# Performance work log

Measured on AMD Instinct MI355X. Metric: run time of the kernel, lower is better.

The kernel has to match this reference:

```python
import jax, jax.numpy as jnp
import numpy as np
from jax import lax


def _conv(x, w, b, pad, dil):
    # standard NCHW conv, OIHW weights
    y = lax.conv_general_dilated(x, w, (1, 1), [(pad, pad), (pad, pad)],
                                 rhs_dilation=(dil, dil),
                                 dimension_numbers=('NCHW', 'OIHW', 'NCHW'))
    return y + b[None, :, None, None]


def _bilinear(img, py, px):
    # img: [B,C,H,W]; py,px: [B,KK,H,W] float sample positions.
    # Zero-padding bilinear sampling (torchvision deform_conv semantics):
    # each of the 4 corners contributes 0 if it lies outside the image.
    B, C, H, W = img.shape
    y0 = jnp.floor(py)
    x0 = jnp.floor(px)
    wy1 = py - y0
    wx1 = px - x0
    imgf = img.reshape(B, C, H * W)

    def corner(yi, xi, wgt):
        valid = (yi >= 0) & (yi <= H - 1) & (xi >= 0) & (xi <= W - 1)
        yc = jnp.clip(yi, 0, H - 1).astype(jnp.int32)
        xc = jnp.clip(xi, 0, W - 1).astype(jnp.int32)
        idx = yc * W + xc  # [B,KK,H,W]
        g = jax.vmap(lambda im, ix: jnp.take(im, ix.reshape(-1), axis=1))(imgf, idx)
        g = g.reshape(B, C, *yi.shape[1:])  # [B,C,KK,H,W]
        return g * (wgt * valid.astype(img.dtype))[:, None]

    return (corner(y0, x0, (1 - wy1) * (1 - wx1))
            + corner(y0, x0 + 1, (1 - wy1) * wx1)
            + corner(y0 + 1, x0, wy1 * (1 - wx1))
            + corner(y0 + 1, x0 + 1, wy1 * wx1))


def _deform_dw(x, off_w, off_b, dw_w, K, pad, dil):
    # offset-predicted deformable depthwise conv (groups == channels)
    B, C, H, W = x.shape
    off = _conv(x, off_w, off_b, pad, dil).reshape(B, K * K, 2, H, W)
    dy, dx = off[:, :, 0], off[:, :, 1]  # torchvision order: (dy, dx) per tap
    ky, kx = jnp.meshgrid(jnp.arange(K), jnp.arange(K), indexing='ij')
    by = (ky.reshape(-1) * dil - pad).astype(x.dtype)  # [KK]
    bx = (kx.reshape(-1) * dil - pad).astype(x.dtype)
    py = jnp.arange(H, dtype=x.dtype)[None, None, :, None] + by[None, :, None, None] + dy
    px = jnp.arange(W, dtype=x.dtype)[None, None, None, :] + bx[None, :, None, None] + dx
    s = _bilinear(x, py, px)  # [B,C,KK,H,W]
    return jnp.einsum('bckhw,ck->bchw', s, dw_w.reshape(C, K * K))


def setup_inputs() -> dict:
    key = jax.random.key(0)
    ks = jax.random.split(key, 9)
    B, C, H, W = 4, 64, 56, 56
    f = lambda k, shape, s: jax.random.normal(k, shape, jnp.float32) * s
    return dict(
        x=f(ks[0], (B, C, H, W), 1.0),
        off_w1=f(ks[1], (2 * 5 * 5, C, 5, 5), 0.01), off_b1=f(ks[2], (2 * 5 * 5,), 0.01),
        dw_w1=f(ks[3], (C, 1, 5, 5), 0.1),
        off_w2=f(ks[4], (2 * 7 * 7, C, 7, 7), 0.01), off_b2=f(ks[5], (2 * 7 * 7,), 0.01),
        dw_w2=f(ks[6], (C, 1, 7, 7), 0.1),
        pw_w=f(ks[7], (C, C, 1, 1), 0.05), pw_b=f(ks[8], (C,), 0.05),
    )


def reference(x, off_w1, off_b1, dw_w1, off_w2, off_b2, dw_w2, pw_w, pw_b):
    attn = _deform_dw(x, off_w1, off_b1, dw_w1, 5, 2, 1)       # 5x5 deformable dw
    attn = _deform_dw(attn, off_w2, off_b2, dw_w2, 7, 9, 3)    # 7x7 dil-3 deformable dw
    attn = _conv(attn, pw_w, pw_b, 0, 1)                       # 1x1 pointwise
    return x * attn                                            # gated multiply
```

## Files before the change

kernel.cpp:

```cpp
#include <hip/hip_runtime.h>

#define BB 4
#define CC 64
#define HH 56
#define WW 56
#define HW (HH*WW)

typedef unsigned short u16;
typedef unsigned int u32;
typedef __attribute__((ext_vector_type(8))) short bf16x8;
typedef __attribute__((ext_vector_type(4))) float f32x4;

__device__ __forceinline__ u16 f2bf(float f) {
    union { float f; unsigned u; } c; c.f = f;
    unsigned u = c.u;
    u = (u + 0x7FFFu + ((u >> 16) & 1u)) >> 16;
    return (u16)u;
}
__device__ __forceinline__ float bf2f(u16 v) {
    union { unsigned u; float f; } c; c.u = ((unsigned)v) << 16;
    return c.f;
}
__device__ __forceinline__ float lo_f(u32 u) {
    union { unsigned u; float f; } c; c.u = u << 16; return c.f;
}
__device__ __forceinline__ float hi_f(u32 u) {
    union { unsigned u; float f; } c; c.u = u & 0xffff0000u; return c.f;
}

#define R1 102400
#define R2 401408
#define R3 4096
#define R4 1600
#define R5 3136
#define TGRID (BB*(HW/64))
#define PREPN (R1+R2+R3+R4+R5)
__global__ __launch_bounds__(256)
void prep_tr_kernel(const float* __restrict__ x,
                    const float* __restrict__ ow1, const float* __restrict__ ow2,
                    const float* __restrict__ pw,  const float* __restrict__ dw1,
                    const float* __restrict__ dw2,
                    u16* __restrict__ xT,
                    u16* __restrict__ w2t1, u16* __restrict__ w2t2,
                    u16* __restrict__ pwT, float* __restrict__ dwT1,
                    float* __restrict__ dwT2) {
    __shared__ u16 tile[64][72];
    const int t = threadIdx.x;
    if (blockIdx.x < TGRID) {
        const int blk = blockIdx.x;
        const int b   = blk / (HW/64);
        const int p0  = (blk % (HW/64))*64;
        const int px  = t & 63, icq = t >> 6;
        const float* ip = x + ((size_t)b*CC + icq*16)*HW + p0 + px;
        #pragma unroll
        for (int i = 0; i < 16; ++i)
            tile[px][icq*16 + i] = f2bf(ip[(size_t)i*HW]);
        __syncthreads();
        const int px2 = t >> 2, g = t & 3;
        u16* op = xT + ((size_t)b*HW + p0 + px2)*64 + g*16;
        const uint4* s = (const uint4*)&tile[px2][g*16];
        ((uint4*)op)[0] = s[0];
        ((uint4*)op)[1] = s[1];
        return;
    }
    const int i = (blockIdx.x - TGRID)*256 + t;
    if (i < R1) {
        const int ic = i & 63, n = (i >> 6) & 63, tap = i >> 12;
        w2t1[i] = f2bf((n < 50) ? ow1[((size_t)n*64 + ic)*25 + tap] : 0.f);
    } else if (i < R1+R2) {
        const int j = i - R1;
        const int ic = j & 63, n = (j >> 6) & 127, tap = j >> 13;
        w2t2[j] = f2bf((n < 98) ? ow2[((size_t)n*64 + ic)*49 + tap] : 0.f);
    } else if (i < R1+R2+R3) {
        const int j = i - (R1+R2);
        pwT[j] = f2bf(pw[j]);
    } else if (i < R1+R2+R3+R4) {
        const int j = i - (R1+R2+R3);
        const int c = j & 63, k = j >> 6;
        dwT1[j] = dw1[c*25 + k];
    } else if (i < R1+R2+R3+R4+R5) {
        const int j = i - (R1+R2+R3+R4);
        const int c = j & 63, k = j >> 6;
        dwT2[j] = dw2[c*49 + k];
    }
}

__device__ __forceinline__ uint4 selz(bool v, uint4 a) {
    const uint4 z = make_uint4(0,0,0,0);
    return v ? a : z;
}

template<int K, int DIL, int PAD, int COUT, int NP, int NPAD, int NTW, int NREAL>
__global__ __launch_bounds__(256, 4)
void conv_mfma_lds_kernel(const u16* __restrict__ xT, const u16* __restrict__ w2t,
                          const float* __restrict__ bias, float* __restrict__ out) {
    constexpr int KK = K*K;
    constexpr int BROWS = 16*NTW;
    __shared__ u16 Ab[2][64*64];
    __shared__ u16 Bb[2][BROWS*64];

    const int nm   = HW/64;
    const int b    = blockIdx.x / nm;
    const int p0   = (blockIdx.x % nm)*64;
    const int nt0  = blockIdx.y;
    const int t    = threadIdx.x;
    const int wave = t >> 6;
    const int lane = t & 63;

    const int spx = t >> 3;
    const int sc  = t & 7;
    const int pA  = p0 + spx;
    const int pB  = p0 + spx + 32;
    const int pyA = pA / WW, pxA = pA % WW;
    const int pyB = pB / WW, pxB = pB % WW;
    const u16* xb = xT + (size_t)b*HW*64;
    const int sslotA = ((sc + spx) & 7)*8;
    const int bn  = t >> 3;
    const int bslot = ((sc + bn) & 7)*8;
    const u16* wbase = w2t + (size_t)nt0*BROWS*64;
    const bool bactive = (BROWS == 32 || bn < BROWS) && (nt0*BROWS + bn < NREAL);

    const int r = lane & 15, quad = lane >> 4;
    const int mloc = wave*16 + r;
    const int arow = mloc*64;
    const int a0s = ((quad     + mloc) & 7)*8;
    const int a1s = ((quad + 4 + mloc) & 7)*8;
    const int b0s = ((quad     + r) & 7)*8;
    const int b1s = ((quad + 4 + r) & 7)*8;

    f32x4 acc[NTW];
    #pragma unroll
    for (int h = 0; h < NTW; ++h) acc[h] = (f32x4){0.f,0.f,0.f,0.f};
    const uint4 z4 = make_uint4(0,0,0,0);

    auto LD = [&](int tap, uint4& a0, uint4& a1, bool& va, bool& vb, uint4& bb) {
        const int dyy = (tap/K)*DIL - PAD;
        const int dxx = (tap%K)*DIL - PAD;
        const int off = dyy*WW + dxx;
        {
            const int yy = pyA + dyy, xx = pxA + dxx;
            va = ((unsigned)yy < (unsigned)HH) && ((unsigned)xx < (unsigned)WW);
            a0 = *(const uint4*)(xb + (size_t)(va ? (pA + off) : 0)*64 + sc*8);
        }
        {
            const int yy = pyB + dyy, xx = pxB + dxx;
            vb = ((unsigned)yy < (unsigned)HH) && ((unsigned)xx < (unsigned)WW);
            a1 = *(const uint4*)(xb + (size_t)(vb ? (pB + off) : 0)*64 + sc*8);
        }
        if (bactive)
            bb = *(const uint4*)(wbase + ((size_t)tap*NP + bn)*64 + sc*8);
    };

    uint4 rA0 = z4, rA1 = z4, rB = z4;
    bool v0 = false, v1 = false;
    LD(0, rA0, rA1, v0, v1, rB);

    #pragma unroll
    for (int tap = 0; tap < KK; ++tap) {
        uint4 nA0 = z4, nA1 = z4, nB = z4;
        bool nv0 = false, nv1 = false;
        if (tap + 1 < KK) LD(tap + 1, nA0, nA1, nv0, nv1, nB);

        u16* A  = &Ab[tap & 1][0];
        u16* Bq = &Bb[tap & 1][0];
        *(uint4*)(A + spx*64      + sslotA) = selz(v0, rA0);
        *(uint4*)(A + (spx+32)*64 + sslotA) = selz(v1, rA1);
        if (bactive) *(uint4*)(Bq + bn*64 + bslot) = rB;
        __syncthreads();

        const bf16x8 av0 = *(const bf16x8*)(A + arow + a0s);
        const bf16x8 av1 = *(const bf16x8*)(A + arow + a1s);
        #pragma unroll
        for (int h = 0; h < NTW; ++h) {
            if (NREAL < NP && nt0*BROWS + h*16 >= NREAL) break;
            const int brow = (h*16 + r)*64;
            const bf16x8 bv0 = *(const bf16x8*)(Bq + brow + b0s);
            const bf16x8 bv1 = *(const bf16x8*)(Bq + brow + b1s);
            acc[h] = __builtin_amdgcn_mfma_f32_16x16x32_bf16(av0, bv0, acc[h], 0, 0, 0);
            acc[h] = __builtin_amdgcn_mfma_f32_16x16x32_bf16(av1, bv1, acc[h], 0, 0, 0);
        }

        rA0 = nA0; rA1 = nA1; rB = nB; v0 = nv0; v1 = nv1;
    }

    #pragma unroll
    for (int h = 0; h < NTW; ++h) {
        const int n = nt0*BROWS + h*16 + r;
        if (n < COUT) {
            const float bv = bias[n];
            float* op = out + ((size_t)b*HW + p0 + wave*16 + quad*4)*NPAD + n;
            #pragma unroll
            for (int r2 = 0; r2 < 4; ++r2) op[(size_t)r2*NPAD] = acc[h][r2] + bv;
        }
    }
}

template<int K, int DIL, int PAD, int NPAD>
__global__ __launch_bounds__(128)
void deform_cl_kernel(const u16* __restrict__ inT, const float* __restrict__ offT,
                      const float* __restrict__ dwT, u16* __restrict__ outT) {
    constexpr int KK = K*K;
    constexpr int PXB = 16;
    __shared__ float4 swt[PXB][KK];
    __shared__ int4   sat[PXB][KK];
    __shared__ float  sdw[KK*64];

    const int t = threadIdx.x;
    const int nbX = (BB*HW/PXB) >> 3;
    const int blk0 = blockIdx.x;
    const int blk = (blk0 & 7)*nbX + (blk0 >> 3);
    const int p0 = blk*PXB;
    const int b  = p0 / HW;
    const int pl0 = p0 - b*HW;

    for (int i = t; i < KK*64; i += 128) sdw[i] = dwT[i];

    for (int i = t; i < PXB*KK; i += 128) {
        const int pix = i / KK, k = i - pix*KK;
        const int pl  = pl0 + pix;
        const int h = pl / WW, w = pl % WW;
        const float* orow = offT + ((size_t)b*HW + pl)*NPAD;
        const float dy = orow[2*k];
        const float dx = orow[2*k+1];
        const float py = (float)(h + (k/K)*DIL - PAD) + dy;
        const float px = (float)(w + (k%K)*DIL - PAD) + dx;
        const float y0f = floorf(py), x0f = floorf(px);
        const float wy1 = py - y0f,  wx1 = px - x0f;
        const float wy0 = 1.f - wy1, wx0 = 1.f - wx1;
        const int y0 = (int)y0f, x0 = (int)x0f;

        const int y0c = min(max(y0,   0), HH-1);
        const int y1c = min(max(y0+1, 0), HH-1);
        const int x0c = min(max(x0,   0), WW-1);
        const int x1c = min(max(x0+1, 0), WW-1);
        const float gy0 = wy0 * ((y0   >= 0 && y0   < HH) ? 1.f : 0.f);
        const float gy1 = wy1 * ((y0+1 >= 0 && y0+1 < HH) ? 1.f : 0.f);
        const float gx0 = wx0 * ((x0   >= 0 && x0   < WW) ? 1.f : 0.f);
        const float gx1 = wx1 * ((x0+1 >= 0 && x0+1 < WW) ? 1.f : 0.f);

        swt[pix][k] = make_float4(gy0*gx0, gy0*gx1, gy1*gx0, gy1*gx1);
        const int r0 = y0c*WW, r1 = y1c*WW;
        sat[pix][k] = make_int4((r0 + x0c) << 7, (r0 + x1c) << 7,
                                (r1 + x0c) << 7, (r1 + x1c) << 7);
    }
    __syncthreads();

    const int lane = t & 63, wave = t >> 6;
    const int pix  = wave*8 + (lane >> 3);
    const int cq   = lane & 7;
    const char* ib = (const char*)(inT + (size_t)b*HW*64) + cq*16;

    float acc[8];
    #pragma unroll
    for (int j = 0; j < 8; ++j) acc[j] = 0.f;

    #pragma unroll 4
    for (int k = 0; k < KK; ++k) {
        const float4 wv = swt[pix][k];
        const int4   av = sat[pix][k];
        const uint4 c00 = *(const uint4*)(ib + av.x);
        const uint4 c01 = *(const uint4*)(ib + av.y);
        const uint4 c10 = *(const uint4*)(ib + av.z);
        const uint4 c11 = *(const uint4*)(ib + av.w);
        const float4 d0 = *(const float4*)&sdw[k*64 + cq*8];
        const float4 d1 = *(const float4*)&sdw[k*64 + cq*8 + 4];
        const float dv[8] = {d0.x,d0.y,d0.z,d0.w,d1.x,d1.y,d1.z,d1.w};
        const u32* p00 = (const u32*)&c00;
        const u32* p01 = (const u32*)&c01;
        const u32* p10 = (const u32*)&c10;
        const u32* p11 = (const u32*)&c11;
        #pragma unroll
        for (int j = 0; j < 4; ++j) {
            const u32 u00 = p00[j], u01 = p01[j], u10 = p10[j], u11 = p11[j];
            const float slo = lo_f(u00)*wv.x + lo_f(u01)*wv.y + lo_f(u10)*wv.z + lo_f(u11)*wv.w;
            const float shi = hi_f(u00)*wv.x + hi_f(u01)*wv.y + hi_f(u10)*wv.z + hi_f(u11)*wv.w;
            acc[2*j]   += slo * dv[2*j];
            acc[2*j+1] += shi * dv[2*j+1];
        }
    }

    uint4 ov;
    u32* ow = (u32*)&ov;
    #pragma unroll
    for (int j = 0; j < 4; ++j)
        ow[j] = (u32)f2bf(acc[2*j]) | ((u32)f2bf(acc[2*j+1]) << 16);
    *(uint4*)((char*)outT + (size_t)(p0 + pix)*128 + cq*16) = ov;
}

__global__ __launch_bounds__(256)
void pw_mfma_kernel(const u16* __restrict__ a2T, const u16* __restrict__ pwT,
                    const float* __restrict__ pb, const float* __restrict__ x,
                    float* __restrict__ out) {
    const int nm = HW/64;
    const int b  = blockIdx.x / nm;
    const int p0 = (blockIdx.x % nm)*64 + (threadIdx.x >> 6)*16;
    const int nt = blockIdx.y;
    const int lane = threadIdx.x & 63;
    const int r = lane & 15, quad = lane >> 4;

    const u16* ap = a2T + ((size_t)b*HW + p0 + r)*64 + quad*8;
    f32x4 acc = (f32x4){0.f,0.f,0.f,0.f};
    #pragma unroll
    for (int ks = 0; ks < 2; ++ks) {
        const bf16x8 av = *(const bf16x8*)(ap + ks*32);
        const bf16x8 bv = *(const bf16x8*)(pwT + ((size_t)(nt*16 + r))*64 + ks*32 + quad*8);
        acc = __builtin_amdgcn_mfma_f32_16x16x32_bf16(av, bv, acc, 0, 0, 0);
    }

    const int n = nt*16 + r;
    const float bv = pb[n];
    const size_t base = ((size_t)b*CC + n)*HW + p0 + quad*4;
    #pragma unroll
    for (int r2 = 0; r2 < 4; ++r2)
        out[base + r2] = x[base + r2] * (acc[r2] + bv);
}

template<int K, int DIL, int PAD, int COUT, int OCB>
__global__ __launch_bounds__(256)
void off_conv_sg_kernel(const float* __restrict__ in, const float* __restrict__ wgt,
                        const float* __restrict__ bias, float* __restrict__ out) {
    constexpr int KK = K*K;
    const int nOB = COUT / OCB;
    const int b   = blockIdx.x / nOB;
    const int oc0 = (blockIdx.x % nOB) * OCB;
    const int x   = threadIdx.x;
    const int h   = blockIdx.y*4 + threadIdx.y;

    float acc[OCB];
    #pragma unroll
    for (int o = 0; o < OCB; ++o) acc[o] = bias[oc0+o];

    const float* inb = in + (size_t)b*CC*HW;
    const float* wb  = wgt + (size_t)oc0*CC*KK;

    for (int ic = 0; ic < CC; ++ic) {
        const float* inp = inb + ic*HW;
        const float* wp  = wb + ic*KK;
        #pragma unroll
        for (int ky = 0; ky < K; ++ky) {
            const int  y  = h + ky*DIL - PAD;
            const bool yv = (y >= 0) && (y < HH);
            const int  yc = yv ? y : 0;
            const float* row = inp + yc*WW;
            #pragma unroll
            for (int kx = 0; kx < K; ++kx) {
                const int  xx = x + kx*DIL - PAD;
                const bool v  = yv && (xx >= 0) && (xx < WW);
                const int  xc = (xx < 0) ? 0 : ((xx >= WW) ? (WW-1) : xx);
                float val = row[xc];
                val = v ? val : 0.f;
                const int t = ky*K + kx;
                #pragma unroll
                for (int o = 0; o < OCB; ++o)
                    acc[o] += wp[(size_t)o*CC*KK + t] * val;
            }
        }
    }

    if (x >= WW) return;
    #pragma unroll
    for (int o = 0; o < OCB; ++o)
        out[((size_t)b*COUT + oc0 + o)*HW + h*WW + x] = acc[o];
}

template<int K, int DIL, int PAD>
__global__ __launch_bounds__(64)
void deform_dw_full_kernel(const float* __restrict__ in, const float* __restrict__ off,
                           const float* __restrict__ dw, float* __restrict__ out) {
    constexpr int KK = K*K;
    const int idx = blockIdx.x*64 + threadIdx.x;
    const int x = idx % WW;
    const int h = (idx / WW) % HH;
    const int c = (idx / HW) % CC;
    const int b = idx / (CC*HW);

    const float* inp  = in  + ((size_t)b*CC + c)*HW;
    const float* offp = off + (size_t)b*(2*KK)*HW + h*WW + x;
    const float* dwp  = dw  + c*KK;

    float acc = 0.f;
    #pragma unroll 7
    for (int k = 0; k < KK; ++k) {
        const float dy = offp[(2*k  )*HW];
        const float dx = offp[(2*k+1)*HW];
        const float py = (float)(h + (k/K)*DIL - PAD) + dy;
        const float px = (float)(x + (k%K)*DIL - PAD) + dx;
        const float y0f = floorf(py), x0f = floorf(px);
        const float wy1 = py - y0f,  wx1 = px - x0f;
        const float wy0 = 1.f - wy1, wx0 = 1.f - wx1;
        const int y0 = (int)y0f, x0 = (int)x0f;

        const int y0c = min(max(y0,   0), HH-1);
        const int y1c = min(max(y0+1, 0), HH-1);
        const int x0c = min(max(x0,   0), WW-1);
        const int x1c = min(max(x0+1, 0), WW-1);
        const float my0 = (y0   >= 0 && y0   < HH) ? 1.f : 0.f;
        const float my1 = (y0+1 >= 0 && y0+1 < HH) ? 1.f : 0.f;
        const float mx0 = (x0   >= 0 && x0   < WW) ? 1.f : 0.f;
        const float mx1 = (x0+1 >= 0 && x0+1 < WW) ? 1.f : 0.f;

        const float v00 = inp[y0c*WW + x0c];
        const float v01 = inp[y0c*WW + x1c];
        const float v10 = inp[y1c*WW + x0c];
        const float v11 = inp[y1c*WW + x1c];

        const float gx0 = wx0*mx0, gx1 = wx1*mx1;
        const float s = (v00*gx0 + v01*gx1) * (wy0*my0)
                      + (v10*gx0 + v11*gx1) * (wy1*my1);
        acc += s * dwp[k];
    }
    out[idx] = acc;
}

__global__ __launch_bounds__(256)
void pw_mul_kernel(const float* __restrict__ x, const float* __restrict__ a2,
                   const float* __restrict__ pw, const float* __restrict__ pb,
                   float* __restrict__ out) {
    constexpr int HW4 = HW/4;
    const int t = blockIdx.x*256 + threadIdx.x;
    if (t >= BB*CC*HW4) return;
    const int sp4 = t % HW4;
    const int oc  = (t / HW4) % CC;
    const int b   = t / (CC*HW4);

    const float4* ap = (const float4*)(a2 + (size_t)b*CC*HW) + sp4;
    const float4* wp4 = (const float4*)(pw + oc*CC);
    const float pbv = pb[oc];
    float4 acc = make_float4(pbv, pbv, pbv, pbv);
    #pragma unroll 4
    for (int ic4 = 0; ic4 < CC/4; ++ic4) {
        const float4 w = wp4[ic4];
        float4 a0 = ap[(ic4*4+0)*HW4];
        float4 a1 = ap[(ic4*4+1)*HW4];
        float4 a2v = ap[(ic4*4+2)*HW4];
        float4 a3 = ap[(ic4*4+3)*HW4];
        acc.x += w.x*a0.x + w.y*a1.x + w.z*a2v.x + w.w*a3.x;
        acc.y += w.x*a0.y + w.y*a1.y + w.z*a2v.y + w.w*a3.y;
        acc.z += w.x*a0.z + w.y*a1.z + w.z*a2v.z + w.w*a3.z;
        acc.w += w.x*a0.w + w.y*a1.w + w.z*a2v.w + w.w*a3.w;
    }
    const float4 xv = ((const float4*)x)[t];
    float4 r;
    r.x = xv.x*acc.x; r.y = xv.y*acc.y; r.z = xv.z*acc.z; r.w = xv.w*acc.w;
    ((float4*)out)[t] = r;
}

extern "C" void kernel_launch(void* const* d_in, const int* in_sizes, int n_in,
                              void* d_out, int out_size, void* d_ws, size_t ws_size,
                              hipStream_t stream) {
    const float* x      = (const float*)d_in[0];
    const float* off_w1 = (const float*)d_in[1];
    const float* off_b1 = (const float*)d_in[2];
    const float* dw_w1  = (const float*)d_in[3];
    const float* off_w2 = (const float*)d_in[4];
    const float* off_b2 = (const float*)d_in[5];
    const float* dw_w2  = (const float*)d_in[6];
    const float* pw_w   = (const float*)d_in[7];
    const float* pw_b   = (const float*)d_in[8];
    float* out = (float*)d_out;

    const size_t nF    = (size_t)BB*CC*HW;
    const size_t attnB = nF*sizeof(float);
    const size_t off2B = (size_t)BB*98*HW*sizeof(float);
    const size_t offTB = (size_t)BB*HW*112*sizeof(float);
    const size_t chB   = (size_t)BB*HW*64*sizeof(u16);
    char* ws = (char*)d_ws;

    const int n    = (int)nF;
    const int dbl  = n/64;
    const int pbl  = (n/4 + 255)/256;
    dim3 cblk(64,4);
    dim3 rgrd1(BB*(50/5), HH/4);
    dim3 rgrd2(BB*(98/7), HH/4);
    dim3 cgrd1(TGRID, 2);
    dim3 cgrd2(TGRID, 4);
    dim3 pgrd(TGRID, 4);
    const int dgrid = BB*HW/16;

    const size_t oOFF  = 0;
    const size_t oXT   = oOFF + offTB;
    const size_t oA1T  = oXT  + chB;
    const size_t oA2T  = oA1T + chB;
    const size_t oW1   = oA2T + chB;
    const size_t oW2   = oW1  + (size_t)R1*2;
    const size_t oPWT  = oW2  + (size_t)R2*2;
    const size_t oDW1  = oPWT + (size_t)R3*2;
    const size_t oDW2  = oDW1 + (size_t)R4*4;
    const size_t TOT   = oDW2 + (size_t)R5*4;

    if (ws_size >= TOT) {
        float* off_buf = (float*)(ws + oOFF);
        u16*   xT      = (u16*)(ws + oXT);
        u16*   a1T     = (u16*)(ws + oA1T);
        u16*   a2T     = (u16*)(ws + oA2T);
        u16*   w2t1    = (u16*)(ws + oW1);
        u16*   w2t2    = (u16*)(ws + oW2);
        u16*   pwT     = (u16*)(ws + oPWT);
        float* dwT1    = (float*)(ws + oDW1);
        float* dwT2    = (float*)(ws + oDW2);

        prep_tr_kernel<<<TGRID + (PREPN+255)/256, 256, 0, stream>>>(
            x, off_w1, off_w2, pw_w, dw_w1, dw_w2,
            xT, w2t1, w2t2, pwT, dwT1, dwT2);

        conv_mfma_lds_kernel<5,1,2,50,64,64,2,64><<<cgrd1, 256, 0, stream>>>(xT, w2t1, off_b1, off_buf);
        deform_cl_kernel<5,1,2,64><<<dgrid, 128, 0, stream>>>(xT, off_buf, dwT1, a1T);

        conv_mfma_lds_kernel<7,3,9,98,128,112,2,112><<<cgrd2, 256, 0, stream>>>(a1T, w2t2, off_b2, off_buf);
        deform_cl_kernel<7,3,9,112><<<dgrid, 128, 0, stream>>>(a1T, off_buf, dwT2, a2T);

        pw_mfma_kernel<<<pgrd, 256, 0, stream>>>(a2T, pwT, pw_b, x, out);
    } else if (ws_size >= off2B + attnB) {
        float* off_buf = (float*)ws;
        float* attn1   = (float*)d_out;
        float* attn2   = (float*)(ws + off2B);
        off_conv_sg_kernel<5,1,2,50,5><<<rgrd1, cblk, 0, stream>>>(x, off_w1, off_b1, off_buf);
        deform_dw_full_kernel<5,1,2><<<dbl, 64, 0, stream>>>(x, off_buf, dw_w1, attn1);
        off_conv_sg_kernel<7,3,9,98,7><<<rgrd2, cblk, 0, stream>>>(attn1, off_w2, off_b2, off_buf);
        deform_dw_full_kernel<7,3,9><<<dbl, 64, 0, stream>>>(attn1, off_buf, dw_w2, attn2);
        pw_mul_kernel<<<pbl, 256, 0, stream>>>(x, attn2, pw_w, pw_b, out);
    } else {
        float* attn1 = (float*)d_out;
        float* attn2 = (float*)ws;
        float* off1  = (float*)ws;
        off_conv_sg_kernel<5,1,2,50,5><<<rgrd1, cblk, 0, stream>>>(x, off_w1, off_b1, off1);
        deform_dw_full_kernel<5,1,2><<<dbl, 64, 0, stream>>>(x, off1, dw_w1, attn1);
        float* off2 = (float*)(ws + attnB);
        off_conv_sg_kernel<7,3,9,98,7><<<rgrd2, cblk, 0, stream>>>(attn1, off_w2, off_b2, off2);
        deform_dw_full_kernel<7,3,9><<<dbl, 64, 0, stream>>>(attn1, off2, dw_w2, attn2);
        pw_mul_kernel<<<pbl, 256, 0, stream>>>(x, attn2, pw_w, pw_b, out);
    }
}
```

Before: 165.1 us.

## Double-buffer per-row bilinear setup in deformable kernel with larger blocks

New measurement: 193.0 us. +16.9%, slower.

```diff
diff --git a/kernel.cpp b/kernel.cpp
--- a/kernel.cpp
+++ b/kernel.cpp
@@ -196,13 +196,15 @@
 }
 
 template<int K, int DIL, int PAD, int NPAD>
-__global__ __launch_bounds__(128)
+__global__ __launch_bounds__(256, 4)
 void deform_cl_kernel(const u16* __restrict__ inT, const float* __restrict__ offT,
                       const float* __restrict__ dwT, u16* __restrict__ outT) {
     constexpr int KK = K*K;
-    constexpr int PXB = 16;
-    __shared__ float4 swt[PXB][KK];
-    __shared__ int4   sat[PXB][KK];
+    constexpr int TC = K;
+    constexpr int NC = K;
+    constexpr int PXB = 32;
+    __shared__ float4 swt[2][PXB*TC];
+    __shared__ int4   sat[2][PXB*TC];
     __shared__ float  sdw[KK*64];
 
     const int t = threadIdx.x;
@@ -213,36 +215,42 @@
     const int b  = p0 / HW;
     const int pl0 = p0 - b*HW;
 
-    for (int i = t; i < KK*64; i += 128) sdw[i] = dwT[i];
-
-    for (int i = t; i < PXB*KK; i += 128) {
-        const int pix = i / KK, k = i - pix*KK;
-        const int pl  = pl0 + pix;
-        const int h = pl / WW, w = pl % WW;
-        const float* orow = offT + ((size_t)b*HW + pl)*NPAD;
-        const float dy = orow[2*k];
-        const float dx = orow[2*k+1];
-        const float py = (float)(h + (k/K)*DIL - PAD) + dy;
-        const float px = (float)(w + (k%K)*DIL - PAD) + dx;
-        const float y0f = floorf(py), x0f = floorf(px);
-        const float wy1 = py - y0f,  wx1 = px - x0f;
-        const float wy0 = 1.f - wy1, wx0 = 1.f - wx1;
-        const int y0 = (int)y0f, x0 = (int)x0f;
-
-        const int y0c = min(max(y0,   0), HH-1);
-        const int y1c = min(max(y0+1, 0), HH-1);
-        const int x0c = min(max(x0,   0), WW-1);
-        const int x1c = min(max(x0+1, 0), WW-1);
-        const float gy0 = wy0 * ((y0   >= 0 && y0   < HH) ? 1.f : 0.f);
-        const float gy1 = wy1 * ((y0+1 >= 0 && y0+1 < HH) ? 1.f : 0.f);
-        const float gx0 = wx0 * ((x0   >= 0 && x0   < WW) ? 1.f : 0.f);
-        const float gx1 = wx1 * ((x0+1 >= 0 && x0+1 < WW) ? 1.f : 0.f);
-
-        swt[pix][k] = make_float4(gy0*gx0, gy0*gx1, gy1*gx0, gy1*gx1);
-        const int r0 = y0c*WW, r1 = y1c*WW;
-        sat[pix][k] = make_int4((r0 + x0c) << 7, (r0 + x1c) << 7,
-                                (r1 + x0c) << 7, (r1 + x1c) << 7);
-    }
+    for (int i = t; i < KK*64; i += 256) sdw[i] = dwT[i];
+
+    auto STAGE = [&](int c) {
+        const int i = t;
+        if (i < PXB*TC) {
+            const int pix = i / TC, kk = i - pix*TC;
+            const int k = c*TC + kk;
+            const int pl  = pl0 + pix;
+            const int h = pl / WW, w = pl % WW;
+            const float* orow = offT + ((size_t)b*HW + pl)*NPAD;
+            const float dy = orow[2*k];
+            const float dx = orow[2*k+1];
+            const float py = (float)(h + (k/K)*DIL - PAD) + dy;
+            const float px = (float)(w + (k%K)*DIL - PAD) + dx;
+            const float y0f = floorf(py), x0f = floorf(px);
+            const float wy1 = py - y0f,  wx1 = px - x0f;
+            const float wy0 = 1.f - wy1, wx0 = 1.f - wx1;
+            const int y0 = (int)y0f, x0 = (int)x0f;
+
+            const int y0c = min(max(y0,   0), HH-1);
+            const int y1c = min(max(y0+1, 0), HH-1);
+            const int x0c = min(max(x0,   0), WW-1);
+            const int x1c = min(max(x0+1, 0), WW-1);
+            const float gy0 = wy0 * ((y0   >= 0 && y0   < HH) ? 1.f : 0.f);
+            const float gy1 = wy1 * ((y0+1 >= 0 && y0+1 < HH) ? 1.f : 0.f);
+            const float gx0 = wx0 * ((x0   >= 0 && x0   < WW) ? 1.f : 0.f);
+            const float gx1 = wx1 * ((x0+1 >= 0 && x0+1 < WW) ? 1.f : 0.f);
+
+            swt[c & 1][pix*TC + kk] = make_float4(gy0*gx0, gy0*gx1, gy1*gx0, gy1*gx1);
+            const int r0 = y0c*WW, r1 = y1c*WW;
+            sat[c & 1][pix*TC + kk] = make_int4((r0 + x0c) << 7, (r0 + x1c) << 7,
+                                                (r1 + x0c) << 7, (r1 + x1c) << 7);
+        }
+    };
+
+    STAGE(0);
     __syncthreads();
 
     const int lane = t & 63, wave = t >> 6;
@@ -254,29 +262,36 @@
     #pragma unroll
     for (int j = 0; j < 8; ++j) acc[j] = 0.f;
 
-    #pragma unroll 4
-    for (int k = 0; k < KK; ++k) {
-        const float4 wv = swt[pix][k];
-        const int4   av = sat[pix][k];
-        const uint4 c00 = *(const uint4*)(ib + av.x);
-        const uint4 c01 = *(const uint4*)(ib + av.y);
-        const uint4 c10 = *(const uint4*)(ib + av.z);
-        const uint4 c11 = *(const uint4*)(ib + av.w);
-        const float4 d0 = *(const float4*)&sdw[k*64 + cq*8];
-        const float4 d1 = *(const float4*)&sdw[k*64 + cq*8 + 4];
-        const float dv[8] = {d0.x,d0.y,d0.z,d0.w,d1.x,d1.y,d1.z,d1.w};
-        const u32* p00 = (const u32*)&c00;
-        const u32* p01 = (const u32*)&c01;
-        const u32* p10 = (const u32*)&c10;
-        const u32* p11 = (const u32*)&c11;
+    for (int c = 0; c < NC; ++c) {
+        if (c + 1 < NC) STAGE(c + 1);
+        const float4* wrow = &swt[c & 1][pix*TC];
+        const int4*   arow = &sat[c & 1][pix*TC];
         #pragma unroll
-        for (int j = 0; j < 4; ++j) {
-            const u32 u00 = p00[j], u01 = p01[j], u10 = p10[j], u11 = p11[j];
-            const float slo = lo_f(u00)*wv.x + lo_f(u01)*wv.y + lo_f(u10)*wv.z + lo_f(u11)*wv.w;
-            const float shi = hi_f(u00)*wv.x + hi_f(u01)*wv.y + hi_f(u10)*wv.z + hi_f(u11)*wv.w;
-            acc[2*j]   += slo * dv[2*j];
-            acc[2*j+1] += shi * dv[2*j+1];
-        }
+        for (int kk = 0; kk < TC; ++kk) {
+            const float4 wv = wrow[kk];
+            const int4   av = arow[kk];
+            const uint4 c00 = *(const uint4*)(ib + av.x);
+            const uint4 c01 = *(const uint4*)(ib + av.y);
+            const uint4 c10 = *(const uint4*)(ib + av.z);
+            const uint4 c11 = *(const uint4*)(ib + av.w);
+            const int k = c*TC + kk;
+            const float4 d0 = *(const float4*)&sdw[k*64 + cq*8];
+            const float4 d1 = *(const float4*)&sdw[k*64 + cq*8 + 4];
+            const float dv[8] = {d0.x,d0.y,d0.z,d0.w,d1.x,d1.y,d1.z,d1.w};
+            const u32* p00 = (const u32*)&c00;
+            const u32* p01 = (const u32*)&c01;
+            const u32* p10 = (const u32*)&c10;
+            const u32* p11 = (const u32*)&c11;
+            #pragma unroll
+            for (int j = 0; j < 4; ++j) {
+                const u32 u00 = p00[j], u01 = p01[j], u10 = p10[j], u11 = p11[j];
+                const float slo = lo_f(u00)*wv.x + lo_f(u01)*wv.y + lo_f(u10)*wv.z + lo_f(u11)*wv.w;
+                const float shi = hi_f(u00)*wv.x + hi_f(u01)*wv.y + hi_f(u10)*wv.z + hi_f(u11)*wv.w;
+                acc[2*j]   += slo * dv[2*j];
+                acc[2*j+1] += shi * dv[2*j+1];
+            }
+        }
+        __syncthreads();
     }
 
     uint4 ov;
@@ -475,7 +490,7 @@
     dim3 cgrd1(TGRID, 2);
     dim3 cgrd2(TGRID, 4);
     dim3 pgrd(TGRID, 4);
-    const int dgrid = BB*HW/16;
+    const int dgrid = BB*HW/32;
 
     const size_t oOFF  = 0;
     const size_t oXT   = oOFF + offTB;
@@ -504,10 +519,10 @@
             xT, w2t1, w2t2, pwT, dwT1, dwT2);
 
         conv_mfma_lds_kernel<5,1,2,50,64,64,2,64><<<cgrd1, 256, 0, stream>>>(xT, w2t1, off_b1, off_buf);
-        deform_cl_kernel<5,1,2,64><<<dgrid, 128, 0, stream>>>(xT, off_buf, dwT1, a1T);
+        deform_cl_kernel<5,1,2,64><<<dgrid, 256, 0, stream>>>(xT, off_buf, dwT1, a1T);
 
         conv_mfma_lds_kernel<7,3,9,98,128,112,2,112><<<cgrd2, 256, 0, stream>>>(a1T, w2t2, off_b2, off_buf);
-        deform_cl_kernel<7,3,9,112><<<dgrid, 128, 0, stream>>>(a1T, off_buf, dwT2, a2T);
+        deform_cl_kernel<7,3,9,112><<<dgrid, 256, 0, stream>>>(a1T, off_buf, dwT2, a2T);
 
         pw_mfma_kernel<<<pgrd, 256, 0, stream>>>(a2T, pwT, pw_b, x, out);
     } else if (ws_size >= off2B + attnB) {
```
